# Kernel tuning notes

Hardware: AMD Instinct MI355X
Metric: run time of the kernel (lower is better)

The kernel has to match this reference:

```python
import jax, jax.numpy as jnp
import numpy as np

N_NODES = 100000
N_EDGES = 1000000
N_GRAPHS = 100
IN_F = 128
HID = 64
N_CLS = 40
EPS = 1e-5


def setup_inputs() -> dict:
    key = jax.random.key(0)
    ks = jax.random.split(key, 16)
    feats = jax.random.normal(ks[0], (N_NODES, IN_F), dtype=jnp.float32)
    src = jax.random.randint(ks[1], (N_EDGES,), 0, N_NODES, dtype=jnp.int32)
    dst = jax.random.randint(ks[2], (N_EDGES,), 0, N_NODES, dtype=jnp.int32)
    offsets = (jnp.arange(N_GRAPHS, dtype=jnp.int32) * (N_NODES // N_GRAPHS))

    def lin(k, fi, fo):
        return jax.random.normal(k, (fi, fo), dtype=jnp.float32) * (fi ** -0.5)

    return {
        "feats": feats, "src": src, "dst": dst, "offsets": offsets,
        "W0": lin(ks[3], IN_F, HID), "b0": jnp.zeros((HID,), jnp.float32),
        "Wr0": lin(ks[4], IN_F, HID), "br0": jnp.zeros((HID,), jnp.float32),
        "g0": jnp.ones((HID,), jnp.float32), "be0": jnp.zeros((HID,), jnp.float32),
        "W1": lin(ks[5], HID, HID), "b1": jnp.zeros((HID,), jnp.float32),
        "Wr1": lin(ks[6], HID, HID), "br1": jnp.zeros((HID,), jnp.float32),
        "g1": jnp.ones((HID,), jnp.float32), "be1": jnp.zeros((HID,), jnp.float32),
        "Wl": lin(ks[7], HID, N_CLS), "bl": jnp.zeros((N_CLS,), jnp.float32),
    }


def _gcn(x, src, dst, W, b):
    """DGL GraphConv, norm='both': D_out^-1/2 A D_in^-1/2 X W + b, then gelu."""
    ones = jnp.ones((src.shape[0],), x.dtype)
    deg_out = jax.ops.segment_sum(ones, src, num_segments=N_NODES)
    deg_in = jax.ops.segment_sum(ones, dst, num_segments=N_NODES)
    dn_out = jnp.where(deg_out > 0, deg_out, 1.0) ** -0.5
    dn_in = jnp.where(deg_in > 0, deg_in, 1.0) ** -0.5
    h = x * dn_out[:, None]
    if W.shape[0] > W.shape[1]:  # weight first (DGL order when in>out)
        h = h @ W
        agg = jax.ops.segment_sum(h[src], dst, num_segments=N_NODES)
        out = agg * dn_in[:, None] + b
    else:
        agg = jax.ops.segment_sum(h[src], dst, num_segments=N_NODES)
        out = (agg * dn_in[:, None]) @ W + b
    return jax.nn.gelu(out, approximate=False)


def _conv_layer(x, src, dst, W, b, Wr, br, g, be):
    new = _gcn(x, src, dst, W, b)
    res = jax.nn.gelu(x @ Wr + br, approximate=False)
    new = new + res
    mean = new.mean(axis=0)
    var = new.var(axis=0)  # biased, like torch BN in training mode
    return (new - mean) * jax.lax.rsqrt(var + EPS) * g + be


def reference(feats, src, dst, offsets, W0, b0, Wr0, br0, g0, be0,
              W1, b1, Wr1, br1, g1, be1, Wl, bl):
    h = _conv_layer(feats, src, dst, W0, b0, Wr0, br0, g0, be0)
    h = _conv_layer(h, src, dst, W1, b1, Wr1, br1, g1, be1)
    # split by graph + pad + take [:, 0]  ==  gather first node of each graph
    first = h[offsets]  # [N_GRAPHS, HID]
    return first @ Wl + bl
```

## Files before the change

kernel.cpp:

```cpp
#include <hip/hip_runtime.h>
#include <hip/hip_bf16.h>
#include <math.h>

#define N_NODES 100000
#define N_EDGES 1000000
#define N_GRAPHS 100
#define IN_F 128
#define HID 64
#define N_CLS 40
#define EPS 1e-5f
#define SB 512
#define SCAN_BLK 391
#define NTILE 1563
#define G1GRID 512

#define HRANGE 32768
#define HNR 4
#define HNC 32
#define HWORDS (HRANGE / 2)
#define HESLICE (N_EDGES / HNC)

#define FRANGE 4096
#define FNR 25

typedef __attribute__((ext_vector_type(8))) short bf16x8;
typedef __attribute__((ext_vector_type(4))) float f32x4;

__device__ __forceinline__ float gelu_exact(float x) {
    return 0.5f * x * (1.0f + erff(x * 0.70710678118654752f));
}

__device__ __forceinline__ unsigned short f2b(float f) {
    unsigned u = __builtin_bit_cast(unsigned, f);
    return (unsigned short)((u + 0x7FFFu + ((u >> 16) & 1u)) >> 16);
}
__device__ __forceinline__ float b2f(unsigned short h) {
    unsigned u = ((unsigned)h) << 16;
    return __builtin_bit_cast(float, u);
}

__global__ void k_prep_w(const float* __restrict__ W0, const float* __restrict__ Wr0,
                         const float* __restrict__ W1, const float* __restrict__ Wr1,
                         unsigned short* __restrict__ Wt0, unsigned short* __restrict__ Wt1) {
    int t = blockIdx.x * 256 + threadIdx.x;
    for (int idx = t; idx < 128 * 128; idx += gridDim.x * 256) {
        int n = idx >> 7, k = idx & 127;
        float v = (n < 64) ? W0[k * 64 + n] : Wr0[k * 64 + (n - 64)];
        Wt0[n * 128 + k] = f2b(v);
    }
    for (int idx = t; idx < 128 * 64; idx += gridDim.x * 256) {
        int n = idx >> 6, k = idx & 63;
        float v = (n < 64) ? W1[k * 64 + n] : Wr1[k * 64 + (n - 64)];
        Wt1[n * 64 + k] = f2b(v);
    }
}

__global__ __launch_bounds__(256) void k_hist(const int* __restrict__ src,
                                              const int* __restrict__ dst,
                                              unsigned* __restrict__ P) {
    __shared__ unsigned h[HWORDS];
    int t = threadIdx.x;
    int b = blockIdx.x;
    int chunk = b & (HNC - 1);
    int job = b >> 5;
    int range = job & (HNR - 1);
    const int* v = (job < HNR) ? dst : src;
    int base = range * HRANGE;
    for (int i = t; i < HWORDS; i += 256) h[i] = 0;
    __syncthreads();
    int e0 = chunk * HESLICE;
    for (int i = t; i < HESLICE / 2; i += 256) {
        uint2 d2 = *(const uint2*)(v + e0 + 2 * i);
        int o = (int)d2.x - base;
        if ((unsigned)o < HRANGE) atomicAdd(&h[o >> 1], 1u << ((o & 1) * 16));
        o = (int)d2.y - base;
        if ((unsigned)o < HRANGE) atomicAdd(&h[o >> 1], 1u << ((o & 1) * 16));
    }
    __syncthreads();
    unsigned* outp = P + (size_t)b * HWORDS;
    for (int i = t; i < HWORDS; i += 256) outp[i] = h[i];
}

__global__ __launch_bounds__(256) void k_hist_reduce(unsigned* __restrict__ P,
                                                     int* __restrict__ cnt_in,
                                                     float* __restrict__ dn_in,
                                                     float* __restrict__ dn_out) {
    int w = blockIdx.x * 256 + threadIdx.x;
    int range = w >> 14;
    int widx = w & (HWORDS - 1);
    unsigned* pin  = P + (size_t)(range * HNC) * HWORDS + widx;
    const unsigned* pout = P + (size_t)((HNR + range) * HNC) * HWORDS + widx;
    unsigned s_in = 0, s_out = 0;
    for (int c = 0; c < HNC; ++c) {
        unsigned v = pin[(size_t)c * HWORDS];
        pin[(size_t)c * HWORDS] = s_in;
        s_in += v;
        s_out += pout[(size_t)c * HWORDS];
    }
    int n0 = range * HRANGE + widx * 2;
    unsigned ci0 = s_in & 0xFFFFu,  ci1 = s_in >> 16;
    unsigned co0 = s_out & 0xFFFFu, co1 = s_out >> 16;
    if (n0 < N_NODES) {
        cnt_in[n0] = (int)ci0;
        dn_in[n0]  = rsqrtf((float)(ci0 > 0 ? ci0 : 1));
        dn_out[n0] = rsqrtf((float)(co0 > 0 ? co0 : 1));
    }
    if (n0 + 1 < N_NODES) {
        cnt_in[n0 + 1] = (int)ci1;
        dn_in[n0 + 1]  = rsqrtf((float)(ci1 > 0 ? ci1 : 1));
        dn_out[n0 + 1] = rsqrtf((float)(co1 > 0 ? co1 : 1));
    }
}

__global__ __launch_bounds__(256) void k_scan_reduce(const int* __restrict__ cnt,
                                                     int* __restrict__ bsum) {
    __shared__ int sh[256];
    int t = threadIdx.x;
    int i = blockIdx.x * 256 + t;
    int c = (i < N_NODES) ? cnt[i] : 0;
    sh[t] = c;
    __syncthreads();
    for (int d = 128; d > 0; d >>= 1) {
        if (t < d) sh[t] += sh[t + d];
        __syncthreads();
    }
    if (t == 0) bsum[blockIdx.x] = sh[0];
}

__global__ __launch_bounds__(512) void k_scan_bsum(const int* __restrict__ bsum,
                                                   int* __restrict__ bpre) {
    __shared__ int sh[512];
    int t = threadIdx.x;
    int v = (t < SCAN_BLK) ? bsum[t] : 0;
    sh[t] = v;
    __syncthreads();
    for (int d = 1; d < 512; d <<= 1) {
        int x = (t >= d) ? sh[t - d] : 0;
        __syncthreads();
        sh[t] += x;
        __syncthreads();
    }
    if (t < SCAN_BLK) bpre[t] = sh[t] - v;
}

__global__ __launch_bounds__(256) void k_scan_write(const int* __restrict__ cnt_in,
                                                    const int* __restrict__ bpre,
                                                    int* __restrict__ row_start) {
    __shared__ int sh[256];
    int t = threadIdx.x;
    int i = blockIdx.x * 256 + t;
    int c = (i < N_NODES) ? cnt_in[i] : 0;
    sh[t] = c;
    __syncthreads();
    for (int d = 1; d < 256; d <<= 1) {
        int v = (t >= d) ? sh[t - d] : 0;
        __syncthreads();
        sh[t] += v;
        __syncthreads();
    }
    int excl = sh[t] - c + bpre[blockIdx.x];
    if (i <= N_NODES) row_start[i] = excl;
}

__global__ __launch_bounds__(256) void k_fill2(const int* __restrict__ src,
                                               const int* __restrict__ dst,
                                               const int* __restrict__ row_start,
                                               const unsigned* __restrict__ Ppre,
                                               int* __restrict__ csr_src) {
    __shared__ unsigned base[FRANGE];
    __shared__ unsigned curs[FRANGE / 2];
    int t = threadIdx.x;
    int b = blockIdx.x;
    int c = b & (HNC - 1);
    int fr = b >> 5;
    int r = fr >> 3;
    int sub = fr & 7;
    int n0 = fr * FRANGE;
    const unsigned* pp = Ppre + (size_t)(r * HNC + c) * HWORDS + sub * (FRANGE / 2);
    for (int i = t; i < FRANGE / 2; i += 256) {
        unsigned pref = pp[i];
        int n = n0 + 2 * i;
        int2 rs = *(const int2*)(row_start + n);
        base[2 * i]     = (n < N_NODES)     ? (unsigned)rs.x + (pref & 0xFFFFu) : 0u;
        base[2 * i + 1] = (n + 1 < N_NODES) ? (unsigned)rs.y + (pref >> 16)     : 0u;
        curs[i] = 0;
    }
    __syncthreads();
    int e0 = c * HESLICE;
    for (int i = t; i < HESLICE / 2; i += 256) {
        uint2 d2 = *(const uint2*)(dst + e0 + 2 * i);
        uint2 s2 = *(const uint2*)(src + e0 + 2 * i);
        int o0 = (int)d2.x - n0;
        if ((unsigned)o0 < FRANGE) {
            unsigned old = atomicAdd(&curs[o0 >> 1], 1u << ((o0 & 1) * 16));
            unsigned loc = (old >> ((o0 & 1) * 16)) & 0xFFFFu;
            csr_src[base[o0] + loc] = (int)s2.x;
        }
        int o1 = (int)d2.y - n0;
        if ((unsigned)o1 < FRANGE) {
            unsigned old = atomicAdd(&curs[o1 >> 1], 1u << ((o1 & 1) * 16));
            unsigned loc = (old >> ((o1 & 1) * 16)) & 0xFFFFu;
            csr_src[base[o1] + loc] = (int)s2.y;
        }
    }
}

__global__ __launch_bounds__(256) void k_gemm0(
    const float* __restrict__ x, const unsigned short* __restrict__ Wt0,
    const float* __restrict__ br0, const float* __restrict__ dn_out,
    unsigned short* __restrict__ h0b, float* __restrict__ res0)
{
    __shared__ unsigned short xs[64][136];
    int t = threadIdx.x;
    int lane = t & 63;
    int w = t >> 6;
    int g = lane >> 4, r16 = lane & 15;

    bf16x8 bfrag[8][4];
    for (int ct = 0; ct < 8; ++ct) {
        int n = ct * 16 + r16;
        for (int ks = 0; ks < 4; ++ks)
            bfrag[ct][ks] = *(const bf16x8*)(Wt0 + n * 128 + ks * 32 + g * 8);
    }
    float br_c[8];
    for (int ct = 4; ct < 8; ++ct) br_c[ct] = br0[(ct - 4) * 16 + r16];

    for (int tile = blockIdx.x; tile < NTILE; tile += gridDim.x) {
        int row0 = tile * 64;
        {
            int rr = t >> 2, q = t & 3;
            int R = row0 + rr;
            bool ok = (R < N_NODES);
            const float* xp = x + (size_t)R * IN_F + q * 32;
            for (int i = 0; i < 8; ++i) {
                float4 v = ok ? *(const float4*)(xp + i * 4) : make_float4(0.f, 0.f, 0.f, 0.f);
                unsigned p0 = (unsigned)f2b(v.x) | ((unsigned)f2b(v.y) << 16);
                unsigned p1 = (unsigned)f2b(v.z) | ((unsigned)f2b(v.w) << 16);
                *(uint2*)(&xs[rr][q * 32 + i * 4]) = make_uint2(p0, p1);
            }
        }
        __syncthreads();

        int arow = w * 16 + r16;
        bf16x8 a[4];
        for (int ks = 0; ks < 4; ++ks)
            a[ks] = *(const bf16x8*)(&xs[arow][ks * 32 + g * 8]);

        f32x4 acc[8];
        for (int ct = 0; ct < 8; ++ct) acc[ct] = (f32x4){0.f, 0.f, 0.f, 0.f};
        for (int ks = 0; ks < 4; ++ks)
            for (int ct = 0; ct < 8; ++ct)
                acc[ct] = __builtin_amdgcn_mfma_f32_16x16x32_bf16(a[ks], bfrag[ct][ks], acc[ct], 0, 0, 0);

        int Rbase = row0 + w * 16 + g * 4;
        float dn[4];
        for (int rg = 0; rg < 4; ++rg) {
            int R = Rbase + rg;
            dn[rg] = (R < N_NODES) ? dn_out[R] : 0.f;
        }
        for (int ct = 0; ct < 8; ++ct) {
            int c = ct * 16 + r16;
            for (int rg = 0; rg < 4; ++rg) {
                int R = Rbase + rg;
                if (R < N_NODES) {
                    if (c < 64) h0b[(size_t)R * 64 + c] = f2b(dn[rg] * acc[ct][rg]);
                    else        res0[(size_t)R * 64 + (c - 64)] = gelu_exact(acc[ct][rg] + br_c[ct]);
                }
            }
        }
        __syncthreads();
    }
}

template <int MODE>
__global__ __launch_bounds__(256) void k_agg(
    const int* __restrict__ row_start, const int* __restrict__ csr_src,
    const unsigned short* __restrict__ hb, const float* __restrict__ dn_in,
    const float* __restrict__ b0, float* __restrict__ out)
{
    int node = blockIdx.x * 4 + (threadIdx.x >> 6);
    int lane = threadIdx.x & 63;
    int sub = lane >> 4, q = lane & 15;
    int beg = row_start[node], end = row_start[node + 1];
    float a0 = 0.f, a1 = 0.f, a2 = 0.f, a3 = 0.f;
    for (int j = beg; j < end; j += 64) {
        int idx = j + lane;
        int eid = (idx < end) ? csr_src[idx] : 0;
        int cnt = end - j; if (cnt > 64) cnt = 64;
        for (int u = sub; u < cnt; u += 4) {
            int s = __shfl(eid, u);
            uint2 v = *(const uint2*)(hb + (size_t)s * 64 + q * 4);
            a0 += b2f((unsigned short)(v.x & 0xFFFFu));
            a1 += b2f((unsigned short)(v.x >> 16));
            a2 += b2f((unsigned short)(v.y & 0xFFFFu));
            a3 += b2f((unsigned short)(v.y >> 16));
        }
    }
    a0 += __shfl_xor(a0, 16); a0 += __shfl_xor(a0, 32);
    a1 += __shfl_xor(a1, 16); a1 += __shfl_xor(a1, 32);
    a2 += __shfl_xor(a2, 16); a2 += __shfl_xor(a2, 32);
    a3 += __shfl_xor(a3, 16); a3 += __shfl_xor(a3, 32);
    if (sub == 0) {
        float dn = dn_in[node];
        size_t o = (size_t)node * 64 + q * 4;
        if (MODE == 0) {
            float4 r = *(const float4*)(out + o);
            float4 wv;
            wv.x = gelu_exact(a0 * dn + b0[q * 4 + 0]) + r.x;
            wv.y = gelu_exact(a1 * dn + b0[q * 4 + 1]) + r.y;
            wv.z = gelu_exact(a2 * dn + b0[q * 4 + 2]) + r.z;
            wv.w = gelu_exact(a3 * dn + b0[q * 4 + 3]) + r.w;
            *(float4*)(out + o) = wv;
        } else {
            float4 wv = make_float4(a0 * dn, a1 * dn, a2 * dn, a3 * dn);
            *(float4*)(out + o) = wv;
        }
    }
}

__global__ __launch_bounds__(256) void k_stats_partial(const float* __restrict__ x,
        double* __restrict__ psum, double* __restrict__ psumsq)
{
    int t = threadIdx.x;
    int c = t & 63, rq = t >> 6;
    int per = (N_NODES + SB - 1) / SB;
    int r0 = blockIdx.x * per;
    int r1 = r0 + per; if (r1 > N_NODES) r1 = N_NODES;
    double s = 0.0, s2 = 0.0;
    for (int r = r0 + rq; r < r1; r += 4) {
        float v = x[(size_t)r * 64 + c];
        s += v; s2 += (double)v * v;
    }
    __shared__ double ls[4][64], ls2[4][64];
    ls[rq][c] = s; ls2[rq][c] = s2;
    __syncthreads();
    if (t < 64) {
        double a = ls[0][t] + ls[1][t] + ls[2][t] + ls[3][t];
        double a2 = ls2[0][t] + ls2[1][t] + ls2[2][t] + ls2[3][t];
        psum[blockIdx.x * 64 + t] = a;
        psumsq[blockIdx.x * 64 + t] = a2;
    }
}

__global__ __launch_bounds__(512) void k_stats_final(const double* __restrict__ psum,
                              const double* __restrict__ psumsq,
                              const float* __restrict__ g, const float* __restrict__ be,
                              float* __restrict__ scale, float* __restrict__ shift)
{
    __shared__ double ls[8][64], ls2[8][64];
    int t = threadIdx.x, c = t & 63, gq = t >> 6;
    double s = 0.0, s2 = 0.0;
    for (int b = gq; b < SB; b += 8) {
        s += psum[b * 64 + c];
        s2 += psumsq[b * 64 + c];
    }
    ls[gq][c] = s; ls2[gq][c] = s2;
    __syncthreads();
    if (t < 64) {
        double a = 0.0, a2 = 0.0;
        for (int i = 0; i < 8; ++i) { a += ls[i][t]; a2 += ls2[i][t]; }
        double mean = a / N_NODES;
        double var = a2 / N_NODES - mean * mean;
        float inv = (float)(1.0 / sqrt(var + (double)EPS)) * g[t];
        scale[t] = inv;
        shift[t] = be[t] - (float)mean * inv;
    }
}

__global__ __launch_bounds__(512) void k_stats_final_f32(const float* __restrict__ psum,
                                  const float* __restrict__ psumsq,
                                  const float* __restrict__ g, const float* __restrict__ be,
                                  float* __restrict__ scale, float* __restrict__ shift)
{
    __shared__ double ls[8][64], ls2[8][64];
    int t = threadIdx.x, c = t & 63, gq = t >> 6;
    double s = 0.0, s2 = 0.0;
    for (int b = gq; b < G1GRID; b += 8) {
        s += (double)psum[b * 64 + c];
        s2 += (double)psumsq[b * 64 + c];
    }
    ls[gq][c] = s; ls2[gq][c] = s2;
    __syncthreads();
    if (t < 64) {
        double a = 0.0, a2 = 0.0;
        for (int i = 0; i < 8; ++i) { a += ls[i][t]; a2 += ls2[i][t]; }
        double mean = a / N_NODES;
        double var = a2 / N_NODES - mean * mean;
        float inv = (float)(1.0 / sqrt(var + (double)EPS)) * g[t];
        scale[t] = inv;
        shift[t] = be[t] - (float)mean * inv;
    }
}

__global__ __launch_bounds__(256) void k_norm1(const float* __restrict__ scale,
                        const float* __restrict__ shift,
                        const float* __restrict__ dn_out,
                        const float* __restrict__ new0, unsigned short* __restrict__ h1b)
{
    int idx = blockIdx.x * 256 + threadIdx.x;
    int r = idx >> 4, q = idx & 15;
    float dn = dn_out[r];
    float4 v = *(const float4*)(new0 + (size_t)r * 64 + q * 4);
    float4 sc = *(const float4*)(scale + q * 4);
    float4 sh = *(const float4*)(shift + q * 4);
    unsigned short h0 = f2b((sc.x * v.x + sh.x) * dn);
    unsigned short h1 = f2b((sc.y * v.y + sh.y) * dn);
    unsigned short h2 = f2b((sc.z * v.z + sh.z) * dn);
    unsigned short h3 = f2b((sc.w * v.w + sh.w) * dn);
    unsigned p0 = (unsigned)h0 | ((unsigned)h1 << 16);
    unsigned p1 = (unsigned)h2 | ((unsigned)h3 << 16);
    *(uint2*)(h1b + (size_t)r * 64 + q * 4) = make_uint2(p0, p1);
}

__global__ __launch_bounds__(256) void k_gemm1(
    const float* __restrict__ aggs, const float* __restrict__ new0,
    const unsigned short* __restrict__ Wt1,
    const float* __restrict__ b1_, const float* __restrict__ br1,
    const float* __restrict__ scale0, const float* __restrict__ shift0,
    float* __restrict__ out_new,
    float* __restrict__ psum1, float* __restrict__ psumsq1)
{
    __shared__ unsigned short xa[64][72];
    __shared__ unsigned short xb[64][72];
    __shared__ float cs[64], cs2[64];
    int t = threadIdx.x;
    int lane = t & 63;
    int w = t >> 6;
    int g = lane >> 4, r16 = lane & 15;

    bf16x8 bW[4][2], bR[4][2];
    for (int ct = 0; ct < 4; ++ct) {
        int n = ct * 16 + r16;
        for (int ks = 0; ks < 2; ++ks) {
            bW[ct][ks] = *(const bf16x8*)(Wt1 + n * 64 + ks * 32 + g * 8);
            bR[ct][ks] = *(const bf16x8*)(Wt1 + (64 + n) * 64 + ks * 32 + g * 8);
        }
    }
    float bias1[4], biasr[4];
    for (int ct = 0; ct < 4; ++ct) {
        bias1[ct] = b1_[ct * 16 + r16];
        biasr[ct] = br1[ct * 16 + r16];
    }
    float4 sc_[4], sh_[4];
    {
        int q = t & 3;
        for (int i = 0; i < 4; ++i) {
            sc_[i] = *(const float4*)(scale0 + q * 16 + i * 4);
            sh_[i] = *(const float4*)(shift0 + q * 16 + i * 4);
        }
    }
    float s_[4] = {0.f, 0.f, 0.f, 0.f}, s2_[4] = {0.f, 0.f, 0.f, 0.f};

    for (int tile = blockIdx.x; tile < NTILE; tile += gridDim.x) {
        int row0 = tile * 64;
        {
            int rr = t >> 2, q = t & 3;
            int R = row0 + rr;
            bool ok = (R < N_NODES);
            const float* pa = aggs + (size_t)R * 64 + q * 16;
            const float* pb = new0 + (size_t)R * 64 + q * 16;
            for (int i = 0; i < 4; ++i) {
                float4 va = ok ? *(const float4*)(pa + i * 4) : make_float4(0.f, 0.f, 0.f, 0.f);
                float4 vb = ok ? *(const float4*)(pb + i * 4) : make_float4(0.f, 0.f, 0.f, 0.f);
                vb.x = sc_[i].x * vb.x + sh_[i].x;
                vb.y = sc_[i].y * vb.y + sh_[i].y;
                vb.z = sc_[i].z * vb.z + sh_[i].z;
                vb.w = sc_[i].w * vb.w + sh_[i].w;
                unsigned pa0 = (unsigned)f2b(va.x) | ((unsigned)f2b(va.y) << 16);
                unsigned pa1 = (unsigned)f2b(va.z) | ((unsigned)f2b(va.w) << 16);
                unsigned pb0 = (unsigned)f2b(vb.x) | ((unsigned)f2b(vb.y) << 16);
                unsigned pb1 = (unsigned)f2b(vb.z) | ((unsigned)f2b(vb.w) << 16);
                *(uint2*)(&xa[rr][q * 16 + i * 4]) = make_uint2(pa0, pa1);
                *(uint2*)(&xb[rr][q * 16 + i * 4]) = make_uint2(pb0, pb1);
            }
        }
        __syncthreads();

        int arow = w * 16 + r16;
        bf16x8 aA[2], aB[2];
        for (int ks = 0; ks < 2; ++ks) {
            aA[ks] = *(const bf16x8*)(&xa[arow][ks * 32 + g * 8]);
            aB[ks] = *(const bf16x8*)(&xb[arow][ks * 32 + g * 8]);
        }
        f32x4 accW[4], accR[4];
        for (int ct = 0; ct < 4; ++ct) {
            accW[ct] = (f32x4){0.f, 0.f, 0.f, 0.f};
            accR[ct] = (f32x4){0.f, 0.f, 0.f, 0.f};
        }
        for (int ks = 0; ks < 2; ++ks)
            for (int ct = 0; ct < 4; ++ct) {
                accW[ct] = __builtin_amdgcn_mfma_f32_16x16x32_bf16(aA[ks], bW[ct][ks], accW[ct], 0, 0, 0);
                accR[ct] = __builtin_amdgcn_mfma_f32_16x16x32_bf16(aB[ks], bR[ct][ks], accR[ct], 0, 0, 0);
            }

        int Rbase = row0 + w * 16 + g * 4;
        for (int ct = 0; ct < 4; ++ct) {
            int c = ct * 16 + r16;
            for (int rg = 0; rg < 4; ++rg) {
                int R = Rbase + rg;
                if (R < N_NODES) {
                    float v = gelu_exact(accW[ct][rg] + bias1[ct]) + gelu_exact(accR[ct][rg] + biasr[ct]);
                    out_new[(size_t)R * 64 + c] = v;
                    s_[ct] += v;
                    s2_[ct] += v * v;
                }
            }
        }
        __syncthreads();
    }

    if (t < 64) { cs[t] = 0.f; cs2[t] = 0.f; }
    __syncthreads();
    for (int ct = 0; ct < 4; ++ct) {
        int c = ct * 16 + r16;
        atomicAdd(&cs[c], s_[ct]);
        atomicAdd(&cs2[c], s2_[ct]);
    }
    __syncthreads();
    if (t < 64) {
        psum1[blockIdx.x * 64 + t] = cs[t];
        psumsq1[blockIdx.x * 64 + t] = cs2[t];
    }
}

__global__ void k_final(const int* __restrict__ offsets,
                        const float* __restrict__ h2,
                        const float* __restrict__ scale, const float* __restrict__ shift,
                        const float* __restrict__ Wl, const float* __restrict__ bl,
                        float* __restrict__ out)
{
    __shared__ float xv[64];
    int g = blockIdx.x;
    int t = threadIdx.x;
    int row = offsets[g];
    if (t < 64) xv[t] = h2[(size_t)row * 64 + t] * scale[t] + shift[t];
    __syncthreads();
    if (t < N_CLS) {
        float s = bl[t];
        for (int k = 0; k < 64; ++k) s += xv[k] * Wl[k * N_CLS + t];
        out[g * N_CLS + t] = s;
    }
}

extern "C" void kernel_launch(void* const* d_in, const int* in_sizes, int n_in,
                              void* d_out, int out_size, void* d_ws, size_t ws_size,
                              hipStream_t stream)
{
    const float* feats = (const float*)d_in[0];
    const int* src     = (const int*)d_in[1];
    const int* dst     = (const int*)d_in[2];
    const int* offsets = (const int*)d_in[3];
    const float* W0  = (const float*)d_in[4];
    const float* b0  = (const float*)d_in[5];
    const float* Wr0 = (const float*)d_in[6];
    const float* br0 = (const float*)d_in[7];
    const float* g0  = (const float*)d_in[8];
    const float* be0 = (const float*)d_in[9];
    const float* W1  = (const float*)d_in[10];
    const float* b1  = (const float*)d_in[11];
    const float* Wr1 = (const float*)d_in[12];
    const float* br1 = (const float*)d_in[13];
    const float* g1  = (const float*)d_in[14];
    const float* be1 = (const float*)d_in[15];
    const float* Wl  = (const float*)d_in[16];
    const float* bl  = (const float*)d_in[17];
    float* out = (float*)d_out;

    char* ws = (char*)d_ws;
    size_t off = 0;
    auto alloc = [&](size_t bytes) -> void* {
        off = (off + 255) & ~(size_t)255;
        void* p = ws + off;
        off += bytes;
        return p;
    };

    const size_t NB = (size_t)N_NODES * HID * sizeof(float);
    unsigned short* Hb = (unsigned short*)alloc(NB / 2);
    float* B = (float*)alloc(NB);
    float* C = (float*)alloc(NB);
    unsigned* P = (unsigned*)C;
    unsigned short* Wt0 = (unsigned short*)alloc(128 * 128 * sizeof(unsigned short));
    unsigned short* Wt1 = (unsigned short*)alloc(128 * 64 * sizeof(unsigned short));
    int* cnt_in = (int*)alloc((size_t)N_NODES * sizeof(int));
    float* dn_out = (float*)alloc(N_NODES * sizeof(float));
    float* dn_in  = (float*)alloc(N_NODES * sizeof(float));
    int* bsum = (int*)alloc(SCAN_BLK * sizeof(int));
    int* bpre = (int*)alloc(SCAN_BLK * sizeof(int));
    int* row_start = (int*)alloc((SCAN_BLK * 256 + 1) * sizeof(int));
    int* csr_src   = (int*)alloc((size_t)N_EDGES * sizeof(int));
    double* psum   = (double*)alloc((size_t)SB * 64 * sizeof(double));
    double* psumsq = (double*)alloc((size_t)SB * 64 * sizeof(double));
    float* psum1   = (float*)alloc((size_t)G1GRID * 64 * sizeof(float));
    float* psumsq1 = (float*)alloc((size_t)G1GRID * 64 * sizeof(float));
    float* scale0 = (float*)alloc(64 * sizeof(float));
    float* shift0 = (float*)alloc(64 * sizeof(float));
    float* scale1 = (float*)alloc(64 * sizeof(float));
    float* shift1 = (float*)alloc(64 * sizeof(float));
    (void)ws_size; (void)n_in; (void)in_sizes; (void)out_size;

    k_prep_w<<<64, 256, 0, stream>>>(W0, Wr0, W1, Wr1, Wt0, Wt1);
    k_hist<<<2 * HNR * HNC, 256, 0, stream>>>(src, dst, P);
    k_hist_reduce<<<HNR * HWORDS / 256, 256, 0, stream>>>(P, cnt_in, dn_in, dn_out);
    k_scan_reduce<<<SCAN_BLK, 256, 0, stream>>>(cnt_in, bsum);
    k_scan_bsum<<<1, 512, 0, stream>>>(bsum, bpre);
    k_scan_write<<<SCAN_BLK, 256, 0, stream>>>(cnt_in, bpre, row_start);
    k_fill2<<<FNR * HNC, 256, 0, stream>>>(src, dst, row_start, P, csr_src);

    k_gemm0<<<512, 256, 0, stream>>>(feats, Wt0, br0, dn_out, Hb, B);
    k_agg<0><<<N_NODES / 4, 256, 0, stream>>>(row_start, csr_src, Hb, dn_in, b0, B);
    k_stats_partial<<<SB, 256, 0, stream>>>(B, psum, psumsq);
    k_stats_final<<<1, 512, 0, stream>>>(psum, psumsq, g0, be0, scale0, shift0);
    k_norm1<<<(N_NODES * HID / 4) / 256, 256, 0, stream>>>(scale0, shift0, dn_out, B, Hb);

    k_agg<1><<<N_NODES / 4, 256, 0, stream>>>(row_start, csr_src, Hb, dn_in, nullptr, C);
    k_gemm1<<<G1GRID, 256, 0, stream>>>(C, B, Wt1, b1, br1, scale0, shift0, C, psum1, psumsq1);
    k_stats_final_f32<<<1, 512, 0, stream>>>(psum1, psumsq1, g1, be1, scale1, shift1);

    k_final<<<N_GRAPHS, 64, 0, stream>>>(offsets, C, scale1, shift1, Wl, bl, out);
}
```

Before: 319.3 us.

## Split GEMM output columns across waves and launch one block per tile

Both MFMA GEMM kernels now give each wave a slice of output columns across all 64 tile rows, instead of all columns for 16 rows. This cuts the per-thread weight fragments and accumulators, which lowers register pressure and can raise occupancy. Grids grow from 512 persistent blocks to one block per tile, and the per-block stats buffers and their final reduction grow to match. The cost is that each wave rereads the A tile from shared memory four times, and blocks no longer reuse weights across tiles.

```diff
diff --git a/kernel.cpp b/kernel.cpp
--- a/kernel.cpp
+++ b/kernel.cpp
@@ -12,7 +12,6 @@
 #define SB 512
 #define SCAN_BLK 391
 #define NTILE 1563
-#define G1GRID 512
 
 #define HRANGE 32768
 #define HNR 4
@@ -215,56 +214,65 @@
     int lane = t & 63;
     int w = t >> 6;
     int g = lane >> 4, r16 = lane & 15;
-
-    bf16x8 bfrag[8][4];
-    for (int ct = 0; ct < 8; ++ct) {
-        int n = ct * 16 + r16;
+    int rr = t >> 2, q4 = t & 3;
+
+    bf16x8 bfrag[2][4];
+    for (int i = 0; i < 2; ++i) {
+        int n = (2 * w + i) * 16 + r16;
         for (int ks = 0; ks < 4; ++ks)
-            bfrag[ct][ks] = *(const bf16x8*)(Wt0 + n * 128 + ks * 32 + g * 8);
-    }
-    float br_c[8];
-    for (int ct = 4; ct < 8; ++ct) br_c[ct] = br0[(ct - 4) * 16 + r16];
+            bfrag[i][ks] = *(const bf16x8*)(Wt0 + n * 128 + ks * 32 + g * 8);
+    }
+    float br_c[2];
+    for (int i = 0; i < 2; ++i) {
+        int c = (2 * w + i) * 16 + r16;
+        br_c[i] = (c >= 64) ? br0[c - 64] : 0.f;
+    }
 
     for (int tile = blockIdx.x; tile < NTILE; tile += gridDim.x) {
         int row0 = tile * 64;
         {
-            int rr = t >> 2, q = t & 3;
             int R = row0 + rr;
             bool ok = (R < N_NODES);
-            const float* xp = x + (size_t)R * IN_F + q * 32;
+            const float* xp = x + (size_t)R * IN_F + q4 * 32;
             for (int i = 0; i < 8; ++i) {
                 float4 v = ok ? *(const float4*)(xp + i * 4) : make_float4(0.f, 0.f, 0.f, 0.f);
                 unsigned p0 = (unsigned)f2b(v.x) | ((unsigned)f2b(v.y) << 16);
                 unsigned p1 = (unsigned)f2b(v.z) | ((unsigned)f2b(v.w) << 16);
-                *(uint2*)(&xs[rr][q * 32 + i * 4]) = make_uint2(p0, p1);
+                *(uint2*)(&xs[rr][q4 * 32 + i * 4]) = make_uint2(p0, p1);
             }
         }
         __syncthreads();
 
-        int arow = w * 16 + r16;
-        bf16x8 a[4];
-        for (int ks = 0; ks < 4; ++ks)
-            a[ks] = *(const bf16x8*)(&xs[arow][ks * 32 + g * 8]);
-
-        f32x4 acc[8];
-        for (int ct = 0; ct < 8; ++ct) acc[ct] = (f32x4){0.f, 0.f, 0.f, 0.f};
-        for (int ks = 0; ks < 4; ++ks)
-            for (int ct = 0; ct < 8; ++ct)
-                acc[ct] = __builtin_amdgcn_mfma_f32_16x16x32_bf16(a[ks], bfrag[ct][ks], acc[ct], 0, 0, 0);
-
-        int Rbase = row0 + w * 16 + g * 4;
-        float dn[4];
-        for (int rg = 0; rg < 4; ++rg) {
-            int R = Rbase + rg;
-            dn[rg] = (R < N_NODES) ? dn_out[R] : 0.f;
-        }
-        for (int ct = 0; ct < 8; ++ct) {
-            int c = ct * 16 + r16;
+        f32x4 acc[4][2];
+        for (int rg16 = 0; rg16 < 4; ++rg16)
+            for (int i = 0; i < 2; ++i)
+                acc[rg16][i] = (f32x4){0.f, 0.f, 0.f, 0.f};
+
+        for (int rg16 = 0; rg16 < 4; ++rg16) {
+            int arow = rg16 * 16 + r16;
+            bf16x8 a[4];
+            for (int ks = 0; ks < 4; ++ks)
+                a[ks] = *(const bf16x8*)(&xs[arow][ks * 32 + g * 8]);
+            for (int ks = 0; ks < 4; ++ks)
+                for (int i = 0; i < 2; ++i)
+                    acc[rg16][i] = __builtin_amdgcn_mfma_f32_16x16x32_bf16(a[ks], bfrag[i][ks], acc[rg16][i], 0, 0, 0);
+        }
+
+        for (int rg16 = 0; rg16 < 4; ++rg16) {
+            int Rbase = row0 + rg16 * 16 + g * 4;
+            float dn[4];
             for (int rg = 0; rg < 4; ++rg) {
                 int R = Rbase + rg;
-                if (R < N_NODES) {
-                    if (c < 64) h0b[(size_t)R * 64 + c] = f2b(dn[rg] * acc[ct][rg]);
-                    else        res0[(size_t)R * 64 + (c - 64)] = gelu_exact(acc[ct][rg] + br_c[ct]);
+                dn[rg] = (R < N_NODES) ? dn_out[R] : 0.f;
+            }
+            for (int i = 0; i < 2; ++i) {
+                int c = (2 * w + i) * 16 + r16;
+                for (int rg = 0; rg < 4; ++rg) {
+                    int R = Rbase + rg;
+                    if (R < N_NODES) {
+                        if (c < 64) h0b[(size_t)R * 64 + c] = f2b(dn[rg] * acc[rg16][i][rg]);
+                        else        res0[(size_t)R * 64 + (c - 64)] = gelu_exact(acc[rg16][i][rg] + br_c[i]);
+                    }
                 }
             }
         }
@@ -375,7 +383,7 @@
     __shared__ double ls[8][64], ls2[8][64];
     int t = threadIdx.x, c = t & 63, gq = t >> 6;
     double s = 0.0, s2 = 0.0;
-    for (int b = gq; b < G1GRID; b += 8) {
+    for (int b = gq; b < NTILE; b += 8) {
         s += (double)psum[b * 64 + c];
         s2 += (double)psumsq[b * 64 + c];
     }
@@ -427,38 +435,34 @@
     int lane = t & 63;
     int w = t >> 6;
     int g = lane >> 4, r16 = lane & 15;
-
-    bf16x8 bW[4][2], bR[4][2];
-    for (int ct = 0; ct < 4; ++ct) {
-        int n = ct * 16 + r16;
+    int rr = t >> 2, q4 = t & 3;
+
+    bf16x8 bW[2], bR[2];
+    {
+        int n = w * 16 + r16;
         for (int ks = 0; ks < 2; ++ks) {
-            bW[ct][ks] = *(const bf16x8*)(Wt1 + n * 64 + ks * 32 + g * 8);
-            bR[ct][ks] = *(const bf16x8*)(Wt1 + (64 + n) * 64 + ks * 32 + g * 8);
-        }
-    }
-    float bias1[4], biasr[4];
-    for (int ct = 0; ct < 4; ++ct) {
-        bias1[ct] = b1_[ct * 16 + r16];
-        biasr[ct] = br1[ct * 16 + r16];
-    }
+            bW[ks] = *(const bf16x8*)(Wt1 + n * 64 + ks * 32 + g * 8);
+            bR[ks] = *(const bf16x8*)(Wt1 + (64 + n) * 64 + ks * 32 + g * 8);
+        }
+    }
+    float bias1 = b1_[w * 16 + r16];
+    float biasr = br1[w * 16 + r16];
     float4 sc_[4], sh_[4];
-    {
-        int q = t & 3;
-        for (int i = 0; i < 4; ++i) {
-            sc_[i] = *(const float4*)(scale0 + q * 16 + i * 4);
-            sh_[i] = *(const float4*)(shift0 + q * 16 + i * 4);
-        }
-    }
-    float s_[4] = {0.f, 0.f, 0.f, 0.f}, s2_[4] = {0.f, 0.f, 0.f, 0.f};
+    for (int i = 0; i < 4; ++i) {
+        sc_[i] = *(const float4*)(scale0 + q4 * 16 + i * 4);
+        sh_[i] = *(const float4*)(shift0 + q4 * 16 + i * 4);
+    }
+    float s_ = 0.f, s2_ = 0.f;
+
+    if (t < 64) { cs[t] = 0.f; cs2[t] = 0.f; }
 
     for (int tile = blockIdx.x; tile < NTILE; tile += gridDim.x) {
         int row0 = tile * 64;
         {
-            int rr = t >> 2, q = t & 3;
             int R = row0 + rr;
             bool ok = (R < N_NODES);
-            const float* pa = aggs + (size_t)R * 64 + q * 16;
-            const float* pb = new0 + (size_t)R * 64 + q * 16;
+            const float* pa = aggs + (size_t)R * 64 + q4 * 16;
+            const float* pb = new0 + (size_t)R * 64 + q4 * 16;
             for (int i = 0; i < 4; ++i) {
                 float4 va = ok ? *(const float4*)(pa + i * 4) : make_float4(0.f, 0.f, 0.f, 0.f);
                 float4 vb = ok ? *(const float4*)(pb + i * 4) : make_float4(0.f, 0.f, 0.f, 0.f);
@@ -470,52 +474,42 @@
                 unsigned pa1 = (unsigned)f2b(va.z) | ((unsigned)f2b(va.w) << 16);
                 unsigned pb0 = (unsigned)f2b(vb.x) | ((unsigned)f2b(vb.y) << 16);
                 unsigned pb1 = (unsigned)f2b(vb.z) | ((unsigned)f2b(vb.w) << 16);
-                *(uint2*)(&xa[rr][q * 16 + i * 4]) = make_uint2(pa0, pa1);
-                *(uint2*)(&xb[rr][q * 16 + i * 4]) = make_uint2(pb0, pb1);
+                *(uint2*)(&xa[rr][q4 * 16 + i * 4]) = make_uint2(pa0, pa1);
+                *(uint2*)(&xb[rr][q4 * 16 + i * 4]) = make_uint2(pb0, pb1);
             }
         }
         __syncthreads();
 
-        int arow = w * 16 + r16;
-        bf16x8 aA[2], aB[2];
-        for (int ks = 0; ks < 2; ++ks) {
-            aA[ks] = *(const bf16x8*)(&xa[arow][ks * 32 + g * 8]);
-            aB[ks] = *(const bf16x8*)(&xb[arow][ks * 32 + g * 8]);
-        }
-        f32x4 accW[4], accR[4];
-        for (int ct = 0; ct < 4; ++ct) {
-            accW[ct] = (f32x4){0.f, 0.f, 0.f, 0.f};
-            accR[ct] = (f32x4){0.f, 0.f, 0.f, 0.f};
-        }
-        for (int ks = 0; ks < 2; ++ks)
-            for (int ct = 0; ct < 4; ++ct) {
-                accW[ct] = __builtin_amdgcn_mfma_f32_16x16x32_bf16(aA[ks], bW[ct][ks], accW[ct], 0, 0, 0);
-                accR[ct] = __builtin_amdgcn_mfma_f32_16x16x32_bf16(aB[ks], bR[ct][ks], accR[ct], 0, 0, 0);
+        int c = w * 16 + r16;
+        for (int rg16 = 0; rg16 < 4; ++rg16) {
+            int arow = rg16 * 16 + r16;
+            bf16x8 aA[2], aB[2];
+            for (int ks = 0; ks < 2; ++ks) {
+                aA[ks] = *(const bf16x8*)(&xa[arow][ks * 32 + g * 8]);
+                aB[ks] = *(const bf16x8*)(&xb[arow][ks * 32 + g * 8]);
             }
-
-        int Rbase = row0 + w * 16 + g * 4;
-        for (int ct = 0; ct < 4; ++ct) {
-            int c = ct * 16 + r16;
+            f32x4 accW = (f32x4){0.f, 0.f, 0.f, 0.f};
+            f32x4 accR = (f32x4){0.f, 0.f, 0.f, 0.f};
+            for (int ks = 0; ks < 2; ++ks) {
+                accW = __builtin_amdgcn_mfma_f32_16x16x32_bf16(aA[ks], bW[ks], accW, 0, 0, 0);
+                accR = __builtin_amdgcn_mfma_f32_16x16x32_bf16(aB[ks], bR[ks], accR, 0, 0, 0);
+            }
+            int Rbase = row0 + rg16 * 16 + g * 4;
             for (int rg = 0; rg < 4; ++rg) {
                 int R = Rbase + rg;
                 if (R < N_NODES) {
-                    float v = gelu_exact(accW[ct][rg] + bias1[ct]) + gelu_exact(accR[ct][rg] + biasr[ct]);
+                    float v = gelu_exact(accW[rg] + bias1) + gelu_exact(accR[rg] + biasr);
                     out_new[(size_t)R * 64 + c] = v;
-                    s_[ct] += v;
-                    s2_[ct] += v * v;
+                    s_ += v;
+                    s2_ += v * v;
                 }
             }
         }
         __syncthreads();
     }
 
-    if (t < 64) { cs[t] = 0.f; cs2[t] = 0.f; }
-    __syncthreads();
-    for (int ct = 0; ct < 4; ++ct) {
-        int c = ct * 16 + r16;
-        atomicAdd(&cs[c], s_[ct]);
-        atomicAdd(&cs2[c], s2_[ct]);
-    }
+    atomicAdd(&cs[w * 16 + r16], s_);
+    atomicAdd(&cs2[w * 16 + r16], s2_);
     __syncthreads();
     if (t < 64) {
         psum1[blockIdx.x * 64 + t] = cs[t];
@@ -591,8 +585,8 @@
     int* csr_src   = (int*)alloc((size_t)N_EDGES * sizeof(int));
     double* psum   = (double*)alloc((size_t)SB * 64 * sizeof(double));
     double* psumsq = (double*)alloc((size_t)SB * 64 * sizeof(double));
-    float* psum1   = (float*)alloc((size_t)G1GRID * 64 * sizeof(float));
-    float* psumsq1 = (float*)alloc((size_t)G1GRID * 64 * sizeof(float));
+    float* psum1   = (float*)alloc((size_t)NTILE * 64 * sizeof(float));
+    float* psumsq1 = (float*)alloc((size_t)NTILE * 64 * sizeof(float));
     float* scale0 = (float*)alloc(64 * sizeof(float));
     float* shift0 = (float*)alloc(64 * sizeof(float));
     float* scale1 = (float*)alloc(64 * sizeof(float));
@@ -607,14 +601,14 @@
     k_scan_write<<<SCAN_BLK, 256, 0, stream>>>(cnt_in, bpre, row_start);
     k_fill2<<<FNR * HNC, 256, 0, stream>>>(src, dst, row_start, P, csr_src);
 
-    k_gemm0<<<512, 256, 0, stream>>>(feats, Wt0, br0, dn_out, Hb, B);
+    k_gemm0<<<NTILE, 256, 0, stream>>>(feats, Wt0, br0, dn_out, Hb, B);
     k_agg<0><<<N_NODES / 4, 256, 0, stream>>>(row_start, csr_src, Hb, dn_in, b0, B);
     k_stats_partial<<<SB, 256, 0, stream>>>(B, psum, psumsq);
     k_stats_final<<<1, 512, 0, stream>>>(psum, psumsq, g0, be0, scale0, shift0);
     k_norm1<<<(N_NODES * HID / 4) / 256, 256, 0, stream>>>(scale0, shift0, dn_out, B, Hb);
 
     k_agg<1><<<N_NODES / 4, 256, 0, stream>>>(row_start, csr_src, Hb, dn_in, nullptr, C);
-    k_gemm1<<<G1GRID, 256, 0, stream>>>(C, B, Wt1, b1, br1, scale0, shift0, C, psum1, psumsq1);
+    k_gemm1<<<NTILE, 256, 0, stream>>>(C, B, Wt1, b1, br1, scale0, shift0, C, psum1, psumsq1);
     k_stats_final_f32<<<1, 512, 0, stream>>>(psum1, psumsq1, g1, be1, scale1, shift1);
 
     k_final<<<N_GRAPHS, 64, 0, stream>>>(offsets, C, scale1, shift1, Wl, bl, out);
```

Result: slower. 341.5 us (+6.9%).
